# Kernel optimization log

Hardware: AMD Instinct MI355X
Metric: run time of the kernel (lower is better)

## Reference

```python
import jax, jax.numpy as jnp
import numpy as np


def setup_inputs() -> dict:
    key = jax.random.key(0)
    k1, k2 = jax.random.split(key)
    B, N, K, Q, D = 8, 20, 5, 15, 1024
    embeddings = jax.random.normal(k1, (B, N, K + Q, D), dtype=jnp.float32)
    # scoring Linear(4*D, 1): weight [1, 4D], bias [1] (init_weight fills bias with 0.01)
    weight = jax.random.normal(k2, (1, 4 * D), dtype=jnp.float32) * 0.02
    bias = jnp.full((1,), 0.01, dtype=jnp.float32)
    return {"embeddings": embeddings, "weight": weight, "bias": bias,
            "N": N, "K": K, "Q": Q}


def reference(embeddings, weight, bias, N, K, Q):
    # embeddings: [B, N, K+Q, D]
    B = embeddings.shape[0]
    D = embeddings.shape[-1]
    emb = embeddings.reshape(B, N, K + Q, D)
    support = emb[:, :, :K, :]                       # [B, N, K, D]
    query = emb[:, :, K:, :].reshape(B, N * Q, D)    # [B, NQ, D]
    proto = support.mean(axis=2)                     # [B, N, D]

    # scoring weight over concat [proto, query, |p-q|, p*q] along last dim:
    # logits = p.w0 + q.w1 + |p-q|.w2 + (p*q).w3 + b  -- same math, no 4D concat
    w = weight.reshape(4, D)
    term_p = jnp.einsum('bnd,d->bn', proto, w[0])[:, None, :]      # [B,1,N]
    term_q = jnp.einsum('bqd,d->bq', query, w[1])[:, :, None]      # [B,NQ,1]
    p = proto[:, None, :, :]                                       # [B,1,N,D]
    q = query[:, :, None, :]                                       # [B,NQ,1,D]
    term_abs = jnp.einsum('bqnd,d->bqn', jnp.abs(p - q), w[2])     # [B,NQ,N]
    term_cos = jnp.einsum('bqd,bnd->bqn', query * w[3], proto)     # [B,NQ,N]
    logits = term_p + term_q + term_abs + term_cos + bias[0]
    return logits
```

## Files before the change

### kernel.cpp

```cpp
#include <hip/hip_runtime.h>

#define DCONST 1024
#define KSUP 5
#define NPROTO 20
#define QPER 15
#define SLOTS (KSUP + QPER)
#define NQ (NPROTO * QPER)
#define NHALF (NPROTO / 2)

__global__ __launch_bounds__(256) void proto_kernel(
    const float* __restrict__ emb,
    const float* __restrict__ weight,
    float* __restrict__ proto,
    float* __restrict__ term_p)
{
    const int bn  = blockIdx.x;
    const int tid = threadIdx.x;
    const int d0  = tid * 4;

    const float* base = emb + ((size_t)bn * SLOTS) * DCONST + d0;
    float4 s = make_float4(0.f, 0.f, 0.f, 0.f);
#pragma unroll
    for (int k = 0; k < KSUP; ++k) {
        float4 v = *reinterpret_cast<const float4*>(base + (size_t)k * DCONST);
        s.x += v.x; s.y += v.y; s.z += v.z; s.w += v.w;
    }
    const float inv = 1.0f / (float)KSUP;
    s.x *= inv; s.y *= inv; s.z *= inv; s.w *= inv;
    *reinterpret_cast<float4*>(proto + (size_t)bn * DCONST + d0) = s;

    float4 w0 = *reinterpret_cast<const float4*>(weight + d0);
    float part = s.x * w0.x + s.y * w0.y + s.z * w0.z + s.w * w0.w;

#pragma unroll
    for (int off = 32; off; off >>= 1) part += __shfl_down(part, off, 64);
    __shared__ float red[4];
    const int wid = tid >> 6;
    if ((tid & 63) == 0) red[wid] = part;
    __syncthreads();
    if (tid == 0) term_p[bn] = red[0] + red[1] + red[2] + red[3];
}

__global__ __launch_bounds__(256, 4) void logits_kernel(
    const float* __restrict__ emb,
    const float* __restrict__ weight,
    const float* __restrict__ bias,
    const float* __restrict__ proto,
    const float* __restrict__ term_p,
    float* __restrict__ out)
{
    const int tid  = threadIdx.x;
    const int lane = tid & 63;
    const int wid  = tid >> 6;
    const int half = blockIdx.x & 1;
    const int grp  = blockIdx.x >> 1;
    const int blocks_per_b = NQ / 4;
    const int b  = grp / blocks_per_b;
    const int qp = (grp % blocks_per_b) * 4 + wid;
    const int nsrc = qp / QPER;
    const int qq   = qp % QPER;

    const float* qrow =
        emb + (((size_t)(b * NPROTO + nsrc) * SLOTS) + KSUP + qq) * DCONST;

    float4 q4[4], w2r[4], qw3[4];
    float tq = 0.f;
#pragma unroll
    for (int j = 0; j < 4; ++j) {
        const int d = j * 256 + lane * 4;
        q4[j]  = *reinterpret_cast<const float4*>(qrow + d);
        w2r[j] = *reinterpret_cast<const float4*>(weight + 2 * DCONST + d);
        float4 w3 = *reinterpret_cast<const float4*>(weight + 3 * DCONST + d);
        float4 w1 = *reinterpret_cast<const float4*>(weight + 1 * DCONST + d);
        qw3[j] = make_float4(q4[j].x * w3.x, q4[j].y * w3.y,
                             q4[j].z * w3.z, q4[j].w * w3.w);
        tq += q4[j].x * w1.x + q4[j].y * w1.y + q4[j].z * w1.z + q4[j].w * w1.w;
    }
#pragma unroll
    for (int off = 32; off; off >>= 1) tq += __shfl_xor(tq, off, 64);
    const float cbase = tq + bias[0];

    const float* pbase = proto + ((size_t)(b * NPROTO) + half * NHALF) * DCONST;

    float acc[NHALF];
#pragma unroll
    for (int n = 0; n < NHALF; ++n) acc[n] = 0.f;

#pragma unroll
    for (int n = 0; n < NHALF; ++n) {
        const float* prow = pbase + (size_t)n * DCONST;
#pragma unroll
        for (int j = 0; j < 4; ++j) {
            const int d = j * 256 + lane * 4;
            float4 p = *reinterpret_cast<const float4*>(prow + d);
            float a = acc[n];
            a = fmaf(fabsf(p.x - q4[j].x), w2r[j].x, a);
            a = fmaf(qw3[j].x, p.x, a);
            a = fmaf(fabsf(p.y - q4[j].y), w2r[j].y, a);
            a = fmaf(qw3[j].y, p.y, a);
            a = fmaf(fabsf(p.z - q4[j].z), w2r[j].z, a);
            a = fmaf(qw3[j].z, p.z, a);
            a = fmaf(fabsf(p.w - q4[j].w), w2r[j].w, a);
            a = fmaf(qw3[j].w, p.w, a);
            acc[n] = a;
        }
    }

    float myval = 0.f;
#pragma unroll
    for (int n = 0; n < NHALF; ++n) {
        float r = acc[n];
#pragma unroll
        for (int off = 32; off; off >>= 1) r += __shfl_xor(r, off, 64);
        if (lane == n) myval = r;
    }

    if (lane < NHALF) {
        const int n = half * NHALF + lane;
        out[((size_t)b * NQ + qp) * NPROTO + n] =
            myval + cbase + term_p[b * NPROTO + n];
    }
}

extern "C" void kernel_launch(void* const* d_in, const int* in_sizes, int n_in,
                              void* d_out, int out_size, void* d_ws, size_t ws_size,
                              hipStream_t stream) {
    const float* emb    = (const float*)d_in[0];
    const float* weight = (const float*)d_in[1];
    const float* bias   = (const float*)d_in[2];
    float* out = (float*)d_out;

    const int B = in_sizes[0] / (NPROTO * SLOTS * DCONST);

    float* proto  = (float*)d_ws;
    float* term_p = proto + (size_t)B * NPROTO * DCONST;

    proto_kernel<<<B * NPROTO, 256, 0, stream>>>(emb, weight, proto, term_p);

    logits_kernel<<<B * (NQ / 4) * 2, 256, 0, stream>>>(emb, weight, bias,
                                                        proto, term_p, out);
}
```

Measured before the change: 84.12 us.

## Fuse prototype computation into logits kernel using shared-memory prototypes

Merges the prototype-mean kernel into the logits kernel. Each block recomputes its half of the prototypes from the support rows into LDS, then processes 12 query rows (3 per wave) against them. The p·w0 term is folded into the inner FMA loop, so the workspace and the separate term_p pass are no longer needed. This removes one launch and the global round-trip for prototypes. The cost is redundant support-row reads in every block and fewer, heavier blocks.

```diff
diff --git a/kernel.cpp b/kernel.cpp
--- a/kernel.cpp
+++ b/kernel.cpp
@@ -7,118 +7,116 @@
 #define SLOTS (KSUP + QPER)
 #define NQ (NPROTO * QPER)
 #define NHALF (NPROTO / 2)
+#define GROWS 12
 
-__global__ __launch_bounds__(256) void proto_kernel(
-    const float* __restrict__ emb,
-    const float* __restrict__ weight,
-    float* __restrict__ proto,
-    float* __restrict__ term_p)
-{
-    const int bn  = blockIdx.x;
-    const int tid = threadIdx.x;
-    const int d0  = tid * 4;
-
-    const float* base = emb + ((size_t)bn * SLOTS) * DCONST + d0;
-    float4 s = make_float4(0.f, 0.f, 0.f, 0.f);
-#pragma unroll
-    for (int k = 0; k < KSUP; ++k) {
-        float4 v = *reinterpret_cast<const float4*>(base + (size_t)k * DCONST);
-        s.x += v.x; s.y += v.y; s.z += v.z; s.w += v.w;
-    }
-    const float inv = 1.0f / (float)KSUP;
-    s.x *= inv; s.y *= inv; s.z *= inv; s.w *= inv;
-    *reinterpret_cast<float4*>(proto + (size_t)bn * DCONST + d0) = s;
-
-    float4 w0 = *reinterpret_cast<const float4*>(weight + d0);
-    float part = s.x * w0.x + s.y * w0.y + s.z * w0.z + s.w * w0.w;
-
-#pragma unroll
-    for (int off = 32; off; off >>= 1) part += __shfl_down(part, off, 64);
-    __shared__ float red[4];
-    const int wid = tid >> 6;
-    if ((tid & 63) == 0) red[wid] = part;
-    __syncthreads();
-    if (tid == 0) term_p[bn] = red[0] + red[1] + red[2] + red[3];
-}
-
-__global__ __launch_bounds__(256, 4) void logits_kernel(
+__global__ __launch_bounds__(256, 2) void relnet_fused_kernel(
     const float* __restrict__ emb,
     const float* __restrict__ weight,
     const float* __restrict__ bias,
-    const float* __restrict__ proto,
-    const float* __restrict__ term_p,
     float* __restrict__ out)
 {
+    __shared__ float sproto[NHALF][DCONST];
+
     const int tid  = threadIdx.x;
     const int lane = tid & 63;
     const int wid  = tid >> 6;
-    const int half = blockIdx.x & 1;
-    const int grp  = blockIdx.x >> 1;
-    const int blocks_per_b = NQ / 4;
-    const int b  = grp / blocks_per_b;
-    const int qp = (grp % blocks_per_b) * 4 + wid;
-    const int nsrc = qp / QPER;
-    const int qq   = qp % QPER;
 
-    const float* qrow =
-        emb + (((size_t)(b * NPROTO + nsrc) * SLOTS) + KSUP + qq) * DCONST;
+    const int groups_per_b = NQ / GROWS;
+    const int b    = blockIdx.x / (2 * groups_per_b);
+    const int rem  = blockIdx.x % (2 * groups_per_b);
+    const int half = rem / groups_per_b;
+    const int grp  = rem % groups_per_b;
 
-    float4 q4[4], w2r[4], qw3[4];
-    float tq = 0.f;
+    float4 w0r[4], w1r[4], w2r[4], w3r[4];
 #pragma unroll
     for (int j = 0; j < 4; ++j) {
         const int d = j * 256 + lane * 4;
-        q4[j]  = *reinterpret_cast<const float4*>(qrow + d);
+        w0r[j] = *reinterpret_cast<const float4*>(weight + 0 * DCONST + d);
+        w1r[j] = *reinterpret_cast<const float4*>(weight + 1 * DCONST + d);
         w2r[j] = *reinterpret_cast<const float4*>(weight + 2 * DCONST + d);
-        float4 w3 = *reinterpret_cast<const float4*>(weight + 3 * DCONST + d);
-        float4 w1 = *reinterpret_cast<const float4*>(weight + 1 * DCONST + d);
-        qw3[j] = make_float4(q4[j].x * w3.x, q4[j].y * w3.y,
-                             q4[j].z * w3.z, q4[j].w * w3.w);
-        tq += q4[j].x * w1.x + q4[j].y * w1.y + q4[j].z * w1.z + q4[j].w * w1.w;
+        w3r[j] = *reinterpret_cast<const float4*>(weight + 3 * DCONST + d);
     }
+    const float bias0 = bias[0];
+
+    const int d0 = tid * 4;
 #pragma unroll
-    for (int off = 32; off; off >>= 1) tq += __shfl_xor(tq, off, 64);
-    const float cbase = tq + bias[0];
-
-    const float* pbase = proto + ((size_t)(b * NPROTO) + half * NHALF) * DCONST;
-
-    float acc[NHALF];
+    for (int n = 0; n < NHALF; ++n) {
+        const float* base =
+            emb + ((size_t)((b * NPROTO + half * NHALF + n) * SLOTS)) * DCONST + d0;
+        float4 s = make_float4(0.f, 0.f, 0.f, 0.f);
 #pragma unroll
-    for (int n = 0; n < NHALF; ++n) acc[n] = 0.f;
+        for (int k = 0; k < KSUP; ++k) {
+            float4 v = *reinterpret_cast<const float4*>(base + (size_t)k * DCONST);
+            s.x += v.x; s.y += v.y; s.z += v.z; s.w += v.w;
+        }
+        s.x *= 0.2f; s.y *= 0.2f; s.z *= 0.2f; s.w *= 0.2f;
+        *reinterpret_cast<float4*>(&sproto[n][d0]) = s;
+    }
+    __syncthreads();
 
 #pragma unroll
-    for (int n = 0; n < NHALF; ++n) {
-        const float* prow = pbase + (size_t)n * DCONST;
+    for (int r = 0; r < 3; ++r) {
+        const int qp   = grp * GROWS + wid * 3 + r;
+        const int nsrc = qp / QPER;
+        const int qq   = qp % QPER;
+        const float* qrow =
+            emb + (((size_t)(b * NPROTO + nsrc) * SLOTS) + KSUP + qq) * DCONST;
+
+        float4 q4[4], qw3[4];
+        float tq = 0.f;
 #pragma unroll
         for (int j = 0; j < 4; ++j) {
             const int d = j * 256 + lane * 4;
-            float4 p = *reinterpret_cast<const float4*>(prow + d);
-            float a = acc[n];
-            a = fmaf(fabsf(p.x - q4[j].x), w2r[j].x, a);
-            a = fmaf(qw3[j].x, p.x, a);
-            a = fmaf(fabsf(p.y - q4[j].y), w2r[j].y, a);
-            a = fmaf(qw3[j].y, p.y, a);
-            a = fmaf(fabsf(p.z - q4[j].z), w2r[j].z, a);
-            a = fmaf(qw3[j].z, p.z, a);
-            a = fmaf(fabsf(p.w - q4[j].w), w2r[j].w, a);
-            a = fmaf(qw3[j].w, p.w, a);
-            acc[n] = a;
+            q4[j] = *reinterpret_cast<const float4*>(qrow + d);
+            qw3[j] = make_float4(q4[j].x * w3r[j].x, q4[j].y * w3r[j].y,
+                                 q4[j].z * w3r[j].z, q4[j].w * w3r[j].w);
+            tq += q4[j].x * w1r[j].x + q4[j].y * w1r[j].y +
+                  q4[j].z * w1r[j].z + q4[j].w * w1r[j].w;
         }
-    }
+#pragma unroll
+        for (int off = 32; off; off >>= 1) tq += __shfl_xor(tq, off, 64);
+        const float cbase = tq + bias0;
 
-    float myval = 0.f;
+        float acc[NHALF];
 #pragma unroll
-    for (int n = 0; n < NHALF; ++n) {
-        float r = acc[n];
+        for (int n = 0; n < NHALF; ++n) acc[n] = 0.f;
+
 #pragma unroll
-        for (int off = 32; off; off >>= 1) r += __shfl_xor(r, off, 64);
-        if (lane == n) myval = r;
-    }
+        for (int n = 0; n < NHALF; ++n) {
+#pragma unroll
+            for (int j = 0; j < 4; ++j) {
+                const float4 p =
+                    *reinterpret_cast<const float4*>(&sproto[n][j * 256 + lane * 4]);
+                float a = acc[n];
+                a = fmaf(fabsf(p.x - q4[j].x), w2r[j].x, a);
+                a = fmaf(qw3[j].x, p.x, a);
+                a = fmaf(p.x, w0r[j].x, a);
+                a = fmaf(fabsf(p.y - q4[j].y), w2r[j].y, a);
+                a = fmaf(qw3[j].y, p.y, a);
+                a = fmaf(p.y, w0r[j].y, a);
+                a = fmaf(fabsf(p.z - q4[j].z), w2r[j].z, a);
+                a = fmaf(qw3[j].z, p.z, a);
+                a = fmaf(p.z, w0r[j].z, a);
+                a = fmaf(fabsf(p.w - q4[j].w), w2r[j].w, a);
+                a = fmaf(qw3[j].w, p.w, a);
+                a = fmaf(p.w, w0r[j].w, a);
+                acc[n] = a;
+            }
+        }
 
-    if (lane < NHALF) {
-        const int n = half * NHALF + lane;
-        out[((size_t)b * NQ + qp) * NPROTO + n] =
-            myval + cbase + term_p[b * NPROTO + n];
+        float myval = 0.f;
+#pragma unroll
+        for (int n = 0; n < NHALF; ++n) {
+            float v = acc[n];
+#pragma unroll
+            for (int off = 32; off; off >>= 1) v += __shfl_xor(v, off, 64);
+            if (lane == n) myval = v;
+        }
+
+        if (lane < NHALF) {
+            out[((size_t)b * NQ + qp) * NPROTO + half * NHALF + lane] =
+                myval + cbase;
+        }
     }
 }
 
@@ -131,12 +129,8 @@
     float* out = (float*)d_out;
 
     const int B = in_sizes[0] / (NPROTO * SLOTS * DCONST);
+    const int groups_per_b = NQ / GROWS;
 
-    float* proto  = (float*)d_ws;
-    float* term_p = proto + (size_t)B * NPROTO * DCONST;
-
-    proto_kernel<<<B * NPROTO, 256, 0, stream>>>(emb, weight, proto, term_p);
-
-    logits_kernel<<<B * (NQ / 4) * 2, 256, 0, stream>>>(emb, weight, bias,
-                                                        proto, term_p, out);
+    relnet_fused_kernel<<<B * 2 * groups_per_b, 256, 0, stream>>>(
+        emb, weight, bias, out);
 }
```

After: 82.51 us. Within noise of the previous version (-1.9%).
